# Optimization experiments

Hardware: AMD Instinct MI355X
Metric: run time of the kernel (lower is better)

The kernel has to match this reference:

```python
import jax, jax.numpy as jnp
import numpy as np

EPS = 1e-5  # torch GroupNorm default

def setup_inputs() -> dict:
    key = jax.random.key(0)
    k1, k2, k3, k4 = jax.random.split(key, 4)
    B = 1048576
    x = jax.random.uniform(k1, (B, 1, 1, 120), dtype=jnp.float32)  # [B,1,1,120]
    conv_w = jax.random.uniform(k2, (120, 1, 1, 120), dtype=jnp.float32, minval=-0.5, maxval=0.5)  # weight_org
    conv_b = jnp.zeros((120,), dtype=jnp.float32)
    gn_w = jnp.ones((120,), dtype=jnp.float32)
    gn_b = jnp.zeros((120,), dtype=jnp.float32)
    lin_w = jax.random.normal(k3, (1, 120), dtype=jnp.float32) * 0.1
    return {"x": x, "conv_w": conv_w, "conv_b": conv_b,
            "gn_w": gn_w, "gn_b": gn_b, "lin_w": lin_w}

def reference(x, conv_w, conv_b, gn_w, gn_b, lin_w):
    # Input binarize: sign(x - 0.5); weight binarize: sign(weight_org)
    xb = jnp.sign(x[:, 0, 0, :] - 0.5)        # [B,120], values in {-1,0,+1}
    wb = jnp.sign(conv_w[:, 0, 0, :])         # [120,120]
    # Conv2d with kernel (1,120) on [B,1,1,120] == GEMM; bias added after
    y = jnp.einsum('bk,ck->bc', xb, wb) + conv_b  # [B,120]
    # GroupNorm(1, 120): normalize over all 120 channels per sample
    mean = jnp.mean(y, axis=1, keepdims=True)
    var = jnp.var(y, axis=1, keepdims=True)
    y = (y - mean) * jax.lax.rsqrt(var + EPS) * gn_w + gn_b
    # Softsign
    y = y / (1.0 + jnp.abs(y))
    # BNNLinear forward: linear(input, weight) -- NO bias used
    out = y @ lin_w.T                          # [B,1]
    return out
```

## Files before the change

### kernel.cpp

```cpp
#include <hip/hip_runtime.h>

#define NCH 120

__global__ void prep_kernel(const float* __restrict__ conv_w,
                            const float* __restrict__ conv_b,
                            const float* __restrict__ gn_w,
                            const float* __restrict__ gn_b,
                            const float* __restrict__ lin_w,
                            unsigned* __restrict__ ws)
{
    __shared__ unsigned s_any;
    if (threadIdx.x == 0) s_any = 0u;
    __syncthreads();
    int c = threadIdx.x;
    if (c < NCH) {
        unsigned sw[4] = {0u,0u,0u,0u};
        unsigned nz[4] = {0u,0u,0u,0u};
        const float* wr = conv_w + c * NCH;
        for (int k = 0; k < NCH; ++k) {
            float w = wr[k];
            unsigned wd = (unsigned)k >> 5, bit = (unsigned)k & 31u;
            sw[wd] |= (w > 0.0f ? 1u : 0u) << bit;
            nz[wd] |= (w != 0.0f ? 1u : 0u) << bit;
        }
        bool anyz = !(nz[0] == 0xFFFFFFFFu && nz[1] == 0xFFFFFFFFu &&
                      nz[2] == 0xFFFFFFFFu && nz[3] == 0x00FFFFFFu);
        if (anyz) atomicOr(&s_any, 1u);
        for (int w = 0; w < 4; ++w) {
            ws[c * 4 + w]       = sw[w];
            ws[480 + c * 4 + w] = nz[w];
        }
        float* cf = (float*)(ws + 960);
        cf[c * 4 + 0] = conv_b[c] - 128.0f;
        cf[c * 4 + 1] = gn_w[c];
        cf[c * 4 + 2] = gn_b[c];
        cf[c * 4 + 3] = lin_w[c];
    }
    __syncthreads();
    if (threadIdx.x == 0) ws[1440] = s_any;
}

__global__ __launch_bounds__(256) void bnn_kernel(
    const float* __restrict__ x,
    const unsigned* __restrict__ ws,
    float* __restrict__ out,
    int B)
{
    __shared__ uint4  sh_sign[NCH];
    __shared__ uint4  sh_nz[NCH];
    __shared__ float4 sh_coef[NCH];
    __shared__ unsigned sh_flag;

    const int tid = threadIdx.x;
    if (tid < NCH) {
        sh_sign[tid] = ((const uint4*)ws)[tid];
        sh_nz[tid]   = ((const uint4*)ws)[120 + tid];
        sh_coef[tid] = ((const float4*)ws)[240 + tid];
    }
    if (tid == 0) sh_flag = ws[1440];
    __syncthreads();

    const int bi = blockIdx.x * 256 + tid;
    if (bi >= B) return;
    const float* __restrict__ xr = x + (long long)bi * NCH;

    unsigned sxa[4] = {0u,0u,0u,0u};
    unsigned minu = 0xFFFFFFFFu;
#pragma unroll
    for (int j = 0; j < 30; ++j) {
        float4 v = *(const float4*)(xr + 4 * j);
        unsigned u0 = __float_as_uint(0.5f - v.x);
        unsigned u1 = __float_as_uint(0.5f - v.y);
        unsigned u2 = __float_as_uint(0.5f - v.z);
        unsigned u3 = __float_as_uint(0.5f - v.w);
        const int w = j >> 3;
        const int p = (j & 7) * 4;
        sxa[w] |= (u0 >> 31) << (p + 0);
        sxa[w] |= (u1 >> 31) << (p + 1);
        sxa[w] |= (u2 >> 31) << (p + 2);
        sxa[w] |= (u3 >> 31) << (p + 3);
        minu = min(minu, min(min(u0, u1), min(u2, u3)));
    }

    const bool fast = (minu != 0u) && (sh_flag == 0u);
    float acc = 0.0f;

    if (fast) {
        unsigned yw[30];
        unsigned sumY = 0u, sumYY = 0u;
#pragma unroll
        for (int c = 0; c < NCH; ++c) {
            uint4 w = sh_sign[c];
            unsigned p = __popc(~(sxa[0] ^ w.x));
            p = __popc(~(sxa[1] ^ w.y)) + p;
            p = __popc(~(sxa[2] ^ w.z)) + p;
            p = __popc(~(sxa[3] ^ w.w)) + p;
            unsigned Y = 2u * p - 8u;
            if ((c & 3) == 0) yw[c >> 2] = Y;
            else              yw[c >> 2] |= Y << ((c & 3) * 8);
            sumY  += Y;
            sumYY += __umul24(Y, Y);
        }
        float meanY = (float)sumY * (1.0f / 120.0f);
        float varY  = (float)sumYY * (1.0f / 120.0f) - meanY * meanY;
        float rstd  = __builtin_amdgcn_rsqf(varY + 1e-5f);
        float nb    = -(meanY - 128.0f) * rstd;
#pragma unroll
        for (int c = 0; c < NCH; ++c) {
            float4 cf = sh_coef[c];
            unsigned Y = (yw[c >> 2] >> ((c & 3) * 8)) & 0xFFu;
            float yf = (float)Y + cf.x;
            float n  = fmaf(yf, rstd, nb);
            float g  = fmaf(n, cf.y, cf.z);
            float s  = g * __builtin_amdgcn_rcpf(1.0f + fabsf(g));
            acc = fmaf(s, cf.w, acc);
        }
    } else {
        unsigned nxa[4] = {0u,0u,0u,0u};
#pragma unroll
        for (int j = 0; j < 30; ++j) {
            float4 v = *(const float4*)(xr + 4 * j);
            unsigned u0 = __float_as_uint(0.5f - v.x);
            unsigned u1 = __float_as_uint(0.5f - v.y);
            unsigned u2 = __float_as_uint(0.5f - v.z);
            unsigned u3 = __float_as_uint(0.5f - v.w);
            const int w = j >> 3;
            const int p = (j & 7) * 4;
            nxa[w] |= (u0 != 0u ? 1u : 0u) << (p + 0);
            nxa[w] |= (u1 != 0u ? 1u : 0u) << (p + 1);
            nxa[w] |= (u2 != 0u ? 1u : 0u) << (p + 2);
            nxa[w] |= (u3 != 0u ? 1u : 0u) << (p + 3);
        }
        unsigned sumY = 0u, sumYY = 0u;
        for (int c = 0; c < NCH; ++c) {
            uint4 w = sh_sign[c];
            uint4 z = sh_nz[c];
            unsigned m0 = nxa[0] & z.x, m1 = nxa[1] & z.y;
            unsigned m2 = nxa[2] & z.z, m3 = nxa[3] & z.w;
            unsigned p = __popc((~(sxa[0] ^ w.x)) & m0)
                       + __popc((~(sxa[1] ^ w.y)) & m1)
                       + __popc((~(sxa[2] ^ w.z)) & m2)
                       + __popc((~(sxa[3] ^ w.w)) & m3);
            unsigned cnt = __popc(m0) + __popc(m1) + __popc(m2) + __popc(m3);
            int Y = 2 * (int)p - (int)cnt + 128;
            sumY  += (unsigned)Y;
            sumYY += (unsigned)(Y * Y);
        }
        float meanY = (float)sumY * (1.0f / 120.0f);
        float varY  = (float)sumYY * (1.0f / 120.0f) - meanY * meanY;
        float rstd  = __builtin_amdgcn_rsqf(varY + 1e-5f);
        float nb    = -(meanY - 128.0f) * rstd;
        for (int c = 0; c < NCH; ++c) {
            uint4 w = sh_sign[c];
            uint4 z = sh_nz[c];
            unsigned m0 = nxa[0] & z.x, m1 = nxa[1] & z.y;
            unsigned m2 = nxa[2] & z.z, m3 = nxa[3] & z.w;
            unsigned p = __popc((~(sxa[0] ^ w.x)) & m0)
                       + __popc((~(sxa[1] ^ w.y)) & m1)
                       + __popc((~(sxa[2] ^ w.z)) & m2)
                       + __popc((~(sxa[3] ^ w.w)) & m3);
            unsigned cnt = __popc(m0) + __popc(m1) + __popc(m2) + __popc(m3);
            int Y = 2 * (int)p - (int)cnt + 128;
            float4 cf = sh_coef[c];
            float yf = (float)Y + cf.x;
            float n  = fmaf(yf, rstd, nb);
            float g  = fmaf(n, cf.y, cf.z);
            float s  = g * __builtin_amdgcn_rcpf(1.0f + fabsf(g));
            acc = fmaf(s, cf.w, acc);
        }
    }
    out[bi] = acc;
}

extern "C" void kernel_launch(void* const* d_in, const int* in_sizes, int n_in,
                              void* d_out, int out_size, void* d_ws, size_t ws_size,
                              hipStream_t stream) {
    const float* x      = (const float*)d_in[0];
    const float* conv_w = (const float*)d_in[1];
    const float* conv_b = (const float*)d_in[2];
    const float* gn_w   = (const float*)d_in[3];
    const float* gn_b   = (const float*)d_in[4];
    const float* lin_w  = (const float*)d_in[5];
    unsigned* ws = (unsigned*)d_ws;
    float* out = (float*)d_out;

    const int B = in_sizes[0] / NCH;
    prep_kernel<<<1, 128, 0, stream>>>(conv_w, conv_b, gn_w, gn_b, lin_w, ws);
    const int grid = (B + 255) / 256;
    bnn_kernel<<<grid, 256, 0, stream>>>(x, ws, out, B);
}
```

Baseline: 173.6 us.

## Load input coalesced per wave and build sign bitmasks via ballot

Each wave now reads its 64 samples' 7680 contiguous floats with lane-strided coalesced loads instead of per-thread strided float4 rows. It packs the sign bits with __ballot into shared memory, and each lane then extracts its own 120-bit mask with shifted word reads. The goal is better global memory coalescing and cache-line use on the main bandwidth-bound load. In exchange it adds ballot and shared-memory traffic. The fallback slow-path decision is now made per wave rather than per thread, and B must be a multiple of 256, since the loads no longer check bounds.

```diff
diff --git a/kernel.cpp b/kernel.cpp
--- a/kernel.cpp
+++ b/kernel.cpp
@@ -49,40 +49,56 @@
     __shared__ uint4  sh_sign[NCH];
     __shared__ uint4  sh_nz[NCH];
     __shared__ float4 sh_coef[NCH];
+    __shared__ unsigned long long s_bal[4][121];
     __shared__ unsigned sh_flag;
 
-    const int tid = threadIdx.x;
+    const int tid  = threadIdx.x;
+    const int lane = tid & 63;
+    const int wv   = tid >> 6;
+
     if (tid < NCH) {
         sh_sign[tid] = ((const uint4*)ws)[tid];
         sh_nz[tid]   = ((const uint4*)ws)[120 + tid];
         sh_coef[tid] = ((const float4*)ws)[240 + tid];
     }
     if (tid == 0) sh_flag = ws[1440];
+
+    const long long wsample0 = (long long)blockIdx.x * 256 + wv * 64;
+    const float* __restrict__ wx = x + wsample0 * NCH;
+    unsigned minu = 0xFFFFFFFFu;
+#pragma unroll
+    for (int j = 0; j < 8; ++j) {
+        float v[15];
+#pragma unroll
+        for (int k = 0; k < 15; ++k)
+            v[k] = wx[(j * 15 + k) * 64 + lane];
+#pragma unroll
+        for (int k = 0; k < 15; ++k) {
+            unsigned u = __float_as_uint(0.5f - v[k]);
+            minu = min(minu, u);
+            unsigned long long b = __ballot(v[k] > 0.5f);
+            if (lane == 0) s_bal[wv][j * 15 + k] = b;
+        }
+    }
+    const bool wave_slow = __any(minu == 0u);
     __syncthreads();
 
-    const int bi = blockIdx.x * 256 + tid;
+    const int bi = (int)wsample0 + lane;
     if (bi >= B) return;
-    const float* __restrict__ xr = x + (long long)bi * NCH;
-
-    unsigned sxa[4] = {0u,0u,0u,0u};
-    unsigned minu = 0xFFFFFFFFu;
-#pragma unroll
-    for (int j = 0; j < 30; ++j) {
-        float4 v = *(const float4*)(xr + 4 * j);
-        unsigned u0 = __float_as_uint(0.5f - v.x);
-        unsigned u1 = __float_as_uint(0.5f - v.y);
-        unsigned u2 = __float_as_uint(0.5f - v.z);
-        unsigned u3 = __float_as_uint(0.5f - v.w);
-        const int w = j >> 3;
-        const int p = (j & 7) * 4;
-        sxa[w] |= (u0 >> 31) << (p + 0);
-        sxa[w] |= (u1 >> 31) << (p + 1);
-        sxa[w] |= (u2 >> 31) << (p + 2);
-        sxa[w] |= (u3 >> 31) << (p + 3);
-        minu = min(minu, min(min(u0, u1), min(u2, u3)));
-    }
-
-    const bool fast = (minu != 0u) && (sh_flag == 0u);
+
+    const unsigned bitpos = (unsigned)lane * 120u;
+    const unsigned widx   = bitpos >> 5;
+    const unsigned sh     = bitpos & 31u;
+    const unsigned* wr = (const unsigned*)&s_bal[wv][0];
+    unsigned t0 = wr[widx], t1 = wr[widx + 1], t2 = wr[widx + 2],
+             t3 = wr[widx + 3], t4 = wr[widx + 4];
+    unsigned sxa[4];
+    sxa[0] = (unsigned)((((unsigned long long)t1 << 32) | t0) >> sh);
+    sxa[1] = (unsigned)((((unsigned long long)t2 << 32) | t1) >> sh);
+    sxa[2] = (unsigned)((((unsigned long long)t3 << 32) | t2) >> sh);
+    sxa[3] = (unsigned)((((unsigned long long)t4 << 32) | t3) >> sh) & 0x00FFFFFFu;
+
+    const bool fast = !wave_slow && (sh_flag == 0u);
     float acc = 0.0f;
 
     if (fast) {
@@ -116,6 +132,7 @@
             acc = fmaf(s, cf.w, acc);
         }
     } else {
+        const float* __restrict__ xr = x + (long long)bi * NCH;
         unsigned nxa[4] = {0u,0u,0u,0u};
 #pragma unroll
         for (int j = 0; j < 30; ++j) {
```

New measurement: 139.0 us. 1.25x faster.

## Replace bit-packed popcount GEMM with int8 MFMA ternary matmul in persistent kernel

Applied to the files above, without the earlier changes.

Inputs and weights are now encoded as int8 ternary values {-1,0,+1}, and the 120x120 product runs on the int8 MFMA 16x16x32 instruction instead of per-thread XOR/popcount loops. Each wave handles 16 samples per tile. Weight fragments stay resident in registers and the grid is a fixed-size persistent launch that loops over tiles. GroupNorm statistics and the softsign-dot output are reduced across lanes with shuffles. This drops the separate fast and slow paths, since zeros are handled natively, at the cost of more register pressure (32 longs of weight fragments) and cross-lane shuffle reductions.

```diff
diff --git a/kernel.cpp b/kernel.cpp
--- a/kernel.cpp
+++ b/kernel.cpp
@@ -1,175 +1,161 @@
 #include <hip/hip_runtime.h>
 
 #define NCH 120
+
+typedef int i32x4 __attribute__((ext_vector_type(4)));
 
 __global__ void prep_kernel(const float* __restrict__ conv_w,
                             const float* __restrict__ conv_b,
                             const float* __restrict__ gn_w,
                             const float* __restrict__ gn_b,
                             const float* __restrict__ lin_w,
-                            unsigned* __restrict__ ws)
+                            unsigned char* __restrict__ wsb)
 {
-    __shared__ unsigned s_any;
-    if (threadIdx.x == 0) s_any = 0u;
-    __syncthreads();
-    int c = threadIdx.x;
-    if (c < NCH) {
-        unsigned sw[4] = {0u,0u,0u,0u};
-        unsigned nz[4] = {0u,0u,0u,0u};
-        const float* wr = conv_w + c * NCH;
-        for (int k = 0; k < NCH; ++k) {
-            float w = wr[k];
-            unsigned wd = (unsigned)k >> 5, bit = (unsigned)k & 31u;
-            sw[wd] |= (w > 0.0f ? 1u : 0u) << bit;
-            nz[wd] |= (w != 0.0f ? 1u : 0u) << bit;
+    const int c = threadIdx.x;
+    if (c >= 128) return;
+    unsigned* row32 = (unsigned*)(wsb + c * 128);
+    for (int kw = 0; kw < 32; ++kw) {
+        unsigned pk = 0u;
+        for (int b = 0; b < 4; ++b) {
+            const int k = kw * 4 + b;
+            unsigned v = 0u;
+            if (c < NCH && k < NCH) {
+                const float w = conv_w[c * NCH + k];
+                v = (w > 0.0f) ? 0x01u : ((w < 0.0f) ? 0xFFu : 0x00u);
+            }
+            pk |= v << (8 * b);
         }
-        bool anyz = !(nz[0] == 0xFFFFFFFFu && nz[1] == 0xFFFFFFFFu &&
-                      nz[2] == 0xFFFFFFFFu && nz[3] == 0x00FFFFFFu);
-        if (anyz) atomicOr(&s_any, 1u);
-        for (int w = 0; w < 4; ++w) {
-            ws[c * 4 + w]       = sw[w];
-            ws[480 + c * 4 + w] = nz[w];
-        }
-        float* cf = (float*)(ws + 960);
-        cf[c * 4 + 0] = conv_b[c] - 128.0f;
-        cf[c * 4 + 1] = gn_w[c];
-        cf[c * 4 + 2] = gn_b[c];
-        cf[c * 4 + 3] = lin_w[c];
+        row32[kw] = pk;
     }
-    __syncthreads();
-    if (threadIdx.x == 0) ws[1440] = s_any;
+    float4* cf = (float4*)(wsb + 16384);
+    float4 o;
+    o.x = (c < NCH) ? conv_b[c] : 0.0f;
+    o.y = (c < NCH) ? gn_w[c]   : 1.0f;
+    o.z = (c < NCH) ? gn_b[c]   : 0.0f;
+    o.w = (c < NCH) ? lin_w[c]  : 0.0f;
+    cf[c] = o;
+}
+
+__device__ __forceinline__ unsigned cvt4(float4 v) {
+    unsigned b0 = (v.x > 0.5f) ? 0x01u : ((v.x < 0.5f) ? 0xFFu : 0x00u);
+    unsigned b1 = (v.y > 0.5f) ? 0x01u : ((v.y < 0.5f) ? 0xFFu : 0x00u);
+    unsigned b2 = (v.z > 0.5f) ? 0x01u : ((v.z < 0.5f) ? 0xFFu : 0x00u);
+    unsigned b3 = (v.w > 0.5f) ? 0x01u : ((v.w < 0.5f) ? 0xFFu : 0x00u);
+    return b0 | (b1 << 8) | (b2 << 16) | (b3 << 24);
 }
 
 __global__ __launch_bounds__(256) void bnn_kernel(
     const float* __restrict__ x,
-    const unsigned* __restrict__ ws,
+    const unsigned char* __restrict__ wsb,
     float* __restrict__ out,
-    int B)
+    int B, int num_tiles, int tiles_per_block)
 {
-    __shared__ uint4  sh_sign[NCH];
-    __shared__ uint4  sh_nz[NCH];
-    __shared__ float4 sh_coef[NCH];
-    __shared__ unsigned sh_flag;
+    __shared__ float4 s_cf[128];
 
-    const int tid = threadIdx.x;
-    if (tid < NCH) {
-        sh_sign[tid] = ((const uint4*)ws)[tid];
-        sh_nz[tid]   = ((const uint4*)ws)[120 + tid];
-        sh_coef[tid] = ((const float4*)ws)[240 + tid];
-    }
-    if (tid == 0) sh_flag = ws[1440];
+    const int tid  = threadIdx.x;
+    const int lane = tid & 63;
+    const int wv   = tid >> 6;
+    const int l15  = lane & 15;
+    const int lg   = lane >> 4;
+
+    if (tid < 128) s_cf[tid] = ((const float4*)(wsb + 16384))[tid];
     __syncthreads();
 
-    const int bi = blockIdx.x * 256 + tid;
-    if (bi >= B) return;
-    const float* __restrict__ xr = x + (long long)bi * NCH;
+    long bfrag[8][4];
+#pragma unroll
+    for (int t = 0; t < 8; ++t)
+#pragma unroll
+        for (int kc = 0; kc < 4; ++kc) {
+            const unsigned char* p = wsb + (t * 16 + l15) * 128 + kc * 32 + lg * 8;
+            bfrag[t][kc] = *(const long*)p;
+        }
 
-    unsigned sxa[4] = {0u,0u,0u,0u};
-    unsigned minu = 0xFFFFFFFFu;
+
+    for (int it = 0; it < tiles_per_block; ++it) {
+        const int tile = blockIdx.x + it * gridDim.x;
+        if (tile >= num_tiles) break;
+        const long long s0 = (long long)tile * 64 + wv * 16;
+
+        long long srow = s0 + l15;
+        if (srow > (long long)B - 1) srow = (long long)B - 1;
+        const float* __restrict__ xr = x + srow * NCH;
+        long afrag[4];
 #pragma unroll
-    for (int j = 0; j < 30; ++j) {
-        float4 v = *(const float4*)(xr + 4 * j);
-        unsigned u0 = __float_as_uint(0.5f - v.x);
-        unsigned u1 = __float_as_uint(0.5f - v.y);
-        unsigned u2 = __float_as_uint(0.5f - v.z);
-        unsigned u3 = __float_as_uint(0.5f - v.w);
-        const int w = j >> 3;
-        const int p = (j & 7) * 4;
-        sxa[w] |= (u0 >> 31) << (p + 0);
-        sxa[w] |= (u1 >> 31) << (p + 1);
-        sxa[w] |= (u2 >> 31) << (p + 2);
-        sxa[w] |= (u3 >> 31) << (p + 3);
-        minu = min(minu, min(min(u0, u1), min(u2, u3)));
-    }
+        for (int kc = 0; kc < 4; ++kc) {
+            const int k0 = kc * 32 + lg * 8;
+            unsigned w0 = 0u, w1 = 0u;
+            if (k0 < NCH) {
+                float4 f0 = *(const float4*)(xr + k0);
+                float4 f1 = *(const float4*)(xr + k0 + 4);
+                w0 = cvt4(f0);
+                w1 = cvt4(f1);
+            }
+            afrag[kc] = (long)(((unsigned long long)w1 << 32) | w0);
+        }
 
-    const bool fast = (minu != 0u) && (sh_flag == 0u);
-    float acc = 0.0f;
+        i32x4 acc[8];
+#pragma unroll
+        for (int t = 0; t < 8; ++t) acc[t] = (i32x4){0, 0, 0, 0};
+#pragma unroll
+        for (int kc = 0; kc < 4; ++kc)
+#pragma unroll
+            for (int t = 0; t < 8; ++t)
+                acc[t] = __builtin_amdgcn_mfma_i32_16x16x32_i8(
+                    afrag[kc], bfrag[t][kc], acc[t], 0, 0, 0);
 
-    if (fast) {
-        unsigned yw[30];
-        unsigned sumY = 0u, sumYY = 0u;
+        int S1[4] = {0, 0, 0, 0};
+        int S2[4] = {0, 0, 0, 0};
 #pragma unroll
-        for (int c = 0; c < NCH; ++c) {
-            uint4 w = sh_sign[c];
-            unsigned p = __popc(~(sxa[0] ^ w.x));
-            p = __popc(~(sxa[1] ^ w.y)) + p;
-            p = __popc(~(sxa[2] ^ w.z)) + p;
-            p = __popc(~(sxa[3] ^ w.w)) + p;
-            unsigned Y = 2u * p - 8u;
-            if ((c & 3) == 0) yw[c >> 2] = Y;
-            else              yw[c >> 2] |= Y << ((c & 3) * 8);
-            sumY  += Y;
-            sumYY += __umul24(Y, Y);
+        for (int t = 0; t < 8; ++t)
+#pragma unroll
+            for (int q = 0; q < 4; ++q) {
+                const int y = acc[t][q];
+                S1[q] += y;
+                S2[q] += y * y;
+            }
+#pragma unroll
+        for (int m = 1; m <= 8; m <<= 1)
+#pragma unroll
+            for (int q = 0; q < 4; ++q) {
+                S1[q] += __shfl_xor(S1[q], m, 64);
+                S2[q] += __shfl_xor(S2[q], m, 64);
+            }
+        float rstd[4], nb[4];
+#pragma unroll
+        for (int q = 0; q < 4; ++q) {
+            const float mean = (float)S1[q] * (1.0f / 120.0f);
+            const float var  = (float)S2[q] * (1.0f / 120.0f) - mean * mean;
+            rstd[q] = __builtin_amdgcn_rsqf(var + 1e-5f);
+            nb[q]   = -mean * rstd[q];
         }
-        float meanY = (float)sumY * (1.0f / 120.0f);
-        float varY  = (float)sumYY * (1.0f / 120.0f) - meanY * meanY;
-        float rstd  = __builtin_amdgcn_rsqf(varY + 1e-5f);
-        float nb    = -(meanY - 128.0f) * rstd;
+
+        float d[4] = {0.0f, 0.0f, 0.0f, 0.0f};
 #pragma unroll
-        for (int c = 0; c < NCH; ++c) {
-            float4 cf = sh_coef[c];
-            unsigned Y = (yw[c >> 2] >> ((c & 3) * 8)) & 0xFFu;
-            float yf = (float)Y + cf.x;
-            float n  = fmaf(yf, rstd, nb);
-            float g  = fmaf(n, cf.y, cf.z);
-            float s  = g * __builtin_amdgcn_rcpf(1.0f + fabsf(g));
-            acc = fmaf(s, cf.w, acc);
+        for (int t = 0; t < 8; ++t) {
+            const float4 cf = s_cf[t * 16 + l15];
+#pragma unroll
+            for (int q = 0; q < 4; ++q) {
+                const float yf = (float)acc[t][q] + cf.x;
+                const float n  = fmaf(yf, rstd[q], nb[q]);
+                const float g  = fmaf(n, cf.y, cf.z);
+                const float s  = g * __builtin_amdgcn_rcpf(1.0f + fabsf(g));
+                d[q] = fmaf(s, cf.w, d[q]);
+            }
         }
-    } else {
-        unsigned nxa[4] = {0u,0u,0u,0u};
 #pragma unroll
-        for (int j = 0; j < 30; ++j) {
-            float4 v = *(const float4*)(xr + 4 * j);
-            unsigned u0 = __float_as_uint(0.5f - v.x);
-            unsigned u1 = __float_as_uint(0.5f - v.y);
-            unsigned u2 = __float_as_uint(0.5f - v.z);
-            unsigned u3 = __float_as_uint(0.5f - v.w);
-            const int w = j >> 3;
-            const int p = (j & 7) * 4;
-            nxa[w] |= (u0 != 0u ? 1u : 0u) << (p + 0);
-            nxa[w] |= (u1 != 0u ? 1u : 0u) << (p + 1);
-            nxa[w] |= (u2 != 0u ? 1u : 0u) << (p + 2);
-            nxa[w] |= (u3 != 0u ? 1u : 0u) << (p + 3);
-        }
-        unsigned sumY = 0u, sumYY = 0u;
-        for (int c = 0; c < NCH; ++c) {
-            uint4 w = sh_sign[c];
-            uint4 z = sh_nz[c];
-            unsigned m0 = nxa[0] & z.x, m1 = nxa[1] & z.y;
-            unsigned m2 = nxa[2] & z.z, m3 = nxa[3] & z.w;
-            unsigned p = __popc((~(sxa[0] ^ w.x)) & m0)
-                       + __popc((~(sxa[1] ^ w.y)) & m1)
-                       + __popc((~(sxa[2] ^ w.z)) & m2)
-                       + __popc((~(sxa[3] ^ w.w)) & m3);
-            unsigned cnt = __popc(m0) + __popc(m1) + __popc(m2) + __popc(m3);
-            int Y = 2 * (int)p - (int)cnt + 128;
-            sumY  += (unsigned)Y;
-            sumYY += (unsigned)(Y * Y);
-        }
-        float meanY = (float)sumY * (1.0f / 120.0f);
-        float varY  = (float)sumYY * (1.0f / 120.0f) - meanY * meanY;
-        float rstd  = __builtin_amdgcn_rsqf(varY + 1e-5f);
-        float nb    = -(meanY - 128.0f) * rstd;
-        for (int c = 0; c < NCH; ++c) {
-            uint4 w = sh_sign[c];
-            uint4 z = sh_nz[c];
-            unsigned m0 = nxa[0] & z.x, m1 = nxa[1] & z.y;
-            unsigned m2 = nxa[2] & z.z, m3 = nxa[3] & z.w;
-            unsigned p = __popc((~(sxa[0] ^ w.x)) & m0)
-                       + __popc((~(sxa[1] ^ w.y)) & m1)
-                       + __popc((~(sxa[2] ^ w.z)) & m2)
-                       + __popc((~(sxa[3] ^ w.w)) & m3);
-            unsigned cnt = __popc(m0) + __popc(m1) + __popc(m2) + __popc(m3);
-            int Y = 2 * (int)p - (int)cnt + 128;
-            float4 cf = sh_coef[c];
-            float yf = (float)Y + cf.x;
-            float n  = fmaf(yf, rstd, nb);
-            float g  = fmaf(n, cf.y, cf.z);
-            float s  = g * __builtin_amdgcn_rcpf(1.0f + fabsf(g));
-            acc = fmaf(s, cf.w, acc);
+        for (int m = 1; m <= 8; m <<= 1)
+#pragma unroll
+            for (int q = 0; q < 4; ++q)
+                d[q] += __shfl_xor(d[q], m, 64);
+
+        if (l15 == 0) {
+#pragma unroll
+            for (int q = 0; q < 4; ++q) {
+                const long long o = s0 + lg * 4 + q;
+                if (o < (long long)B) out[o] = d[q];
+            }
         }
     }
-    out[bi] = acc;
 }
 
 extern "C" void kernel_launch(void* const* d_in, const int* in_sizes, int n_in,
@@ -181,11 +167,14 @@
     const float* gn_w   = (const float*)d_in[3];
     const float* gn_b   = (const float*)d_in[4];
     const float* lin_w  = (const float*)d_in[5];
-    unsigned* ws = (unsigned*)d_ws;
+    unsigned char* wsb = (unsigned char*)d_ws;
     float* out = (float*)d_out;
 
     const int B = in_sizes[0] / NCH;
-    prep_kernel<<<1, 128, 0, stream>>>(conv_w, conv_b, gn_w, gn_b, lin_w, ws);
-    const int grid = (B + 255) / 256;
-    bnn_kernel<<<grid, 256, 0, stream>>>(x, ws, out, B);
+    prep_kernel<<<1, 128, 0, stream>>>(conv_w, conv_b, gn_w, gn_b, lin_w, wsb);
+
+    const int num_tiles = (B + 63) / 64;
+    const int grid = 2048;
+    const int tiles_per_block = (num_tiles + grid - 1) / grid;
+    bnn_kernel<<<grid, 256, 0, stream>>>(x, wsb, out, B, num_tiles, tiles_per_block);
 }
```

New measurement: 154.3 us. 11.2% less time.
